# Kernel tuning notes

Hardware: AMD Instinct MI355X
Metric: run time of the kernel (lower is better)

## Reference

```python
import jax, jax.numpy as jnp
import numpy as np

LN_EPS = 1e-5


def _layer_norm(x, w, b, eps=LN_EPS):
    mu = jnp.mean(x, axis=-1, keepdims=True)
    var = jnp.var(x, axis=-1, keepdims=True)
    return (x - mu) * jax.lax.rsqrt(var + eps) * w + b


def setup_inputs() -> dict:
    key = jax.random.key(0)
    ks = jax.random.split(key, 6)
    H, I, B, S = 1024, 4096, 4, 2048
    return {
        "x": jax.random.normal(ks[0], (B, S, H), jnp.float32),
        "ln_weight": jnp.ones((H,), jnp.float32),
        "ln_bias": jnp.zeros((H,), jnp.float32),
        "i2h_weight": jax.random.normal(ks[1], (2 * I, H), jnp.float32) * 0.02,
        "i2h_bias": jax.random.normal(ks[2], (2 * I,), jnp.float32) * 0.02,
        "h2o_weight": jax.random.normal(ks[3], (H, I), jnp.float32) * 0.02,
        "h2o_bias": jax.random.normal(ks[4], (H,), jnp.float32) * 0.02,
        "post_ln_weight": jnp.ones((H,), jnp.float32),
        "post_ln_bias": jnp.zeros((H,), jnp.float32),
    }


def reference(x, ln_weight, ln_bias, i2h_weight, i2h_bias, h2o_weight, h2o_bias,
              post_ln_weight, post_ln_bias):
    B, S, H = x.shape
    x2 = x.reshape(-1, H)  # [N, H]
    x_ln = _layer_norm(x2, ln_weight, ln_bias)
    # i2h: [N, 2I]
    pre = jnp.einsum('nh,oh->no', x_ln, i2h_weight) + i2h_bias
    I = pre.shape[-1] // 2
    pre_gate, lin = pre[:, :I], pre[:, I:]
    # gated gelu (tanh-approx, matching gelu_fused)
    hid = jax.nn.gelu(pre_gate, approximate=True) * lin
    out = jnp.einsum('ni,oi->no', hid, h2o_weight) + h2o_bias
    out = _layer_norm(out, post_ln_weight, post_ln_bias)
    out = out + x2  # residual (dropout=0)
    return out.reshape(B, S, H)
```

## Files before the change

### kernel.cpp

```cpp
#include <hip/hip_runtime.h>
#include <stdint.h>

#define N_ROWS 8192
#define H_DIM  1024
#define I_DIM  4096

typedef unsigned short u16;
typedef __bf16 bf16x8 __attribute__((ext_vector_type(8)));
typedef float f32x4 __attribute__((ext_vector_type(4)));
typedef u16 u16x4 __attribute__((ext_vector_type(4)));

__device__ __forceinline__ u16 f2bf(float f) {
    union { float f; uint32_t u; } v; v.f = f;
    uint32_t u = v.u;
    u += 0x7FFFu + ((u >> 16) & 1u);
    return (u16)(u >> 16);
}

__device__ __forceinline__ float bf2f(u16 h) {
    union { uint32_t u; float f; } v; v.u = ((uint32_t)h) << 16;
    return v.f;
}

__device__ __forceinline__ float gelu_tanh(float x) {
    float u = 0.7978845608028654f * (x + 0.044715f * x * x * x);
    u = fminf(fmaxf(u, -15.f), 15.f);
    float e = __expf(2.f * u);
    float t = (e - 1.f) / (e + 1.f);
    return 0.5f * x * (1.f + t);
}

__device__ __forceinline__ void load_lds16(const void* g, void* l) {
    auto gp = reinterpret_cast<const __attribute__((address_space(1))) uint32_t*>(
        reinterpret_cast<uintptr_t>(g));
    auto lp = reinterpret_cast<__attribute__((address_space(3))) uint32_t*>(
        static_cast<uint32_t>(reinterpret_cast<uintptr_t>(l)));
    __builtin_amdgcn_global_load_lds(gp, lp, 16, 0, 0);
}

__device__ __forceinline__ void stage_tile(const u16* __restrict__ src, int stride,
                                           int row0, int k0, u16* lds, int t) {
#pragma unroll
    for (int i = 0; i < 2; ++i) {
        int r = i * 64 + (t >> 2);
        int s = t & 3;
        int ss = s ^ (r & 3);
        const u16* g = src + (size_t)(row0 + r) * stride + k0 + ss * 8;
        load_lds16(g, lds + i * 2048 + t * 8);
    }
}

__device__ __forceinline__ bf16x8 ld_frag(const u16* lds, int row, int g) {
    int slot = g ^ (row & 3);
    return *reinterpret_cast<const bf16x8*>(lds + row * 32 + slot * 8);
}

__global__ __launch_bounds__(256, 2) void gemm1_gated(
    const u16* __restrict__ A, const u16* __restrict__ W,
    const float* __restrict__ bias, u16* __restrict__ hid)
{
    __shared__ u16 As[2][128 * 32];
    __shared__ u16 Bg[2][128 * 32];
    __shared__ u16 Bl[2][128 * 32];
    const int t = threadIdx.x;
    const int lane = t & 63, wid = t >> 6;
    const int wm = wid >> 1, wn = wid & 1;
    const int row0 = blockIdx.y * 128, c0 = blockIdx.x * 128;
    const int g = lane >> 4, r16 = lane & 15;

    f32x4 accg[4][4] = {};
    f32x4 accl[4][4] = {};

    stage_tile(A, H_DIM, row0, 0, As[0], t);
    stage_tile(W, H_DIM, c0, 0, Bg[0], t);
    stage_tile(W, H_DIM, I_DIM + c0, 0, Bl[0], t);

    const int NT = H_DIM / 32;
    for (int kt = 0; kt < NT; ++kt) {
        const int cur = kt & 1;
        __syncthreads();
        if (kt + 1 < NT) {
            const int k0 = (kt + 1) * 32;
            stage_tile(A, H_DIM, row0, k0, As[cur ^ 1], t);
            stage_tile(W, H_DIM, c0, k0, Bg[cur ^ 1], t);
            stage_tile(W, H_DIM, I_DIM + c0, k0, Bl[cur ^ 1], t);
        }
        bf16x8 af[4], bgf[4], blf[4];
#pragma unroll
        for (int m = 0; m < 4; ++m) af[m] = ld_frag(As[cur], wm * 64 + m * 16 + r16, g);
#pragma unroll
        for (int n = 0; n < 4; ++n) {
            bgf[n] = ld_frag(Bg[cur], wn * 64 + n * 16 + r16, g);
            blf[n] = ld_frag(Bl[cur], wn * 64 + n * 16 + r16, g);
        }
#pragma unroll
        for (int m = 0; m < 4; ++m)
#pragma unroll
            for (int n = 0; n < 4; ++n) {
                accg[m][n] = __builtin_amdgcn_mfma_f32_16x16x32_bf16(af[m], bgf[n], accg[m][n], 0, 0, 0);
                accl[m][n] = __builtin_amdgcn_mfma_f32_16x16x32_bf16(af[m], blf[n], accl[m][n], 0, 0, 0);
            }
    }

#pragma unroll
    for (int m = 0; m < 4; ++m)
#pragma unroll
        for (int n = 0; n < 4; ++n) {
            const int cg = c0 + wn * 64 + n * 16 + r16;
            const float bgv = bias[cg], blv = bias[I_DIM + cg];
#pragma unroll
            for (int r = 0; r < 4; ++r) {
                const int row = row0 + wm * 64 + m * 16 + g * 4 + r;
                float gate = accg[m][n][r] + bgv;
                float lin  = accl[m][n][r] + blv;
                hid[(size_t)row * I_DIM + cg] = f2bf(gelu_tanh(gate) * lin);
            }
        }
}

__global__ __launch_bounds__(256, 2) void gemm2_k(
    const u16* __restrict__ A, const u16* __restrict__ W,
    const float* __restrict__ bias, u16* __restrict__ opb)
{
    __shared__ u16 As[2][128 * 32];
    __shared__ u16 Bs[2][128 * 32];
    const int t = threadIdx.x;
    const int lane = t & 63, wid = t >> 6;
    const int wm = wid >> 1, wn = wid & 1;
    const int row0 = blockIdx.y * 128, c0 = blockIdx.x * 128;
    const int g = lane >> 4, r16 = lane & 15;

    f32x4 acc[4][4] = {};

    stage_tile(A, I_DIM, row0, 0, As[0], t);
    stage_tile(W, I_DIM, c0, 0, Bs[0], t);

    const int NT = I_DIM / 32;
    for (int kt = 0; kt < NT; ++kt) {
        const int cur = kt & 1;
        __syncthreads();
        if (kt + 1 < NT) {
            const int k0 = (kt + 1) * 32;
            stage_tile(A, I_DIM, row0, k0, As[cur ^ 1], t);
            stage_tile(W, I_DIM, c0, k0, Bs[cur ^ 1], t);
        }
        bf16x8 af[4], bf[4];
#pragma unroll
        for (int m = 0; m < 4; ++m) af[m] = ld_frag(As[cur], wm * 64 + m * 16 + r16, g);
#pragma unroll
        for (int n = 0; n < 4; ++n) bf[n] = ld_frag(Bs[cur], wn * 64 + n * 16 + r16, g);
#pragma unroll
        for (int m = 0; m < 4; ++m)
#pragma unroll
            for (int n = 0; n < 4; ++n)
                acc[m][n] = __builtin_amdgcn_mfma_f32_16x16x32_bf16(af[m], bf[n], acc[m][n], 0, 0, 0);
    }

#pragma unroll
    for (int m = 0; m < 4; ++m)
#pragma unroll
        for (int n = 0; n < 4; ++n) {
            const int cg = c0 + wn * 64 + n * 16 + r16;
            const float bv = bias[cg];
#pragma unroll
            for (int r = 0; r < 4; ++r) {
                const int row = row0 + wm * 64 + m * 16 + g * 4 + r;
                opb[(size_t)row * H_DIM + cg] = f2bf(acc[m][n][r] + bv);
            }
        }
}

__device__ __forceinline__ void block_mean_var(float s, float s2, float* red, int t,
                                               float& mu, float& var) {
#pragma unroll
    for (int off = 32; off > 0; off >>= 1) {
        s  += __shfl_down(s, off);
        s2 += __shfl_down(s2, off);
    }
    const int wid = t >> 6;
    if ((t & 63) == 0) { red[wid] = s; red[4 + wid] = s2; }
    __syncthreads();
    if (t == 0) {
        float a = red[0] + red[1] + red[2] + red[3];
        float b = red[4] + red[5] + red[6] + red[7];
        red[0] = a * (1.f / H_DIM);
        red[1] = b * (1.f / H_DIM);
    }
    __syncthreads();
    mu = red[0];
    var = red[1] - mu * mu;
}

__global__ void ln_pre(const float* __restrict__ x, const float* __restrict__ w,
                       const float* __restrict__ b, u16* __restrict__ xln)
{
    __shared__ float red[8];
    const int row = blockIdx.x, t = threadIdx.x;
    const float4 v = reinterpret_cast<const float4*>(x + (size_t)row * H_DIM)[t];
    float mu, var;
    block_mean_var(v.x + v.y + v.z + v.w,
                   v.x * v.x + v.y * v.y + v.z * v.z + v.w * v.w, red, t, mu, var);
    const float rstd = rsqrtf(var + 1e-5f);
    const float4 wv = reinterpret_cast<const float4*>(w)[t];
    const float4 bv = reinterpret_cast<const float4*>(b)[t];
    u16x4 o;
    o.x = f2bf((v.x - mu) * rstd * wv.x + bv.x);
    o.y = f2bf((v.y - mu) * rstd * wv.y + bv.y);
    o.z = f2bf((v.z - mu) * rstd * wv.z + bv.z);
    o.w = f2bf((v.w - mu) * rstd * wv.w + bv.w);
    reinterpret_cast<u16x4*>(xln + (size_t)row * H_DIM)[t] = o;
}

__global__ void ln_post_res(const u16* __restrict__ op, const float* __restrict__ w,
                            const float* __restrict__ b, const float* __restrict__ x,
                            float* __restrict__ out)
{
    __shared__ float red[8];
    const int row = blockIdx.x, t = threadIdx.x;
    const u16x4 hv = reinterpret_cast<const u16x4*>(op + (size_t)row * H_DIM)[t];
    float4 v;
    v.x = bf2f(hv.x); v.y = bf2f(hv.y); v.z = bf2f(hv.z); v.w = bf2f(hv.w);
    float mu, var;
    block_mean_var(v.x + v.y + v.z + v.w,
                   v.x * v.x + v.y * v.y + v.z * v.z + v.w * v.w, red, t, mu, var);
    const float rstd = rsqrtf(var + 1e-5f);
    const float4 wv = reinterpret_cast<const float4*>(w)[t];
    const float4 bv = reinterpret_cast<const float4*>(b)[t];
    const float4 xv = reinterpret_cast<const float4*>(x + (size_t)row * H_DIM)[t];
    float4 o;
    o.x = (v.x - mu) * rstd * wv.x + bv.x + xv.x;
    o.y = (v.y - mu) * rstd * wv.y + bv.y + xv.y;
    o.z = (v.z - mu) * rstd * wv.z + bv.z + xv.z;
    o.w = (v.w - mu) * rstd * wv.w + bv.w + xv.w;
    reinterpret_cast<float4*>(out + (size_t)row * H_DIM)[t] = o;
}

__global__ void cvt_bf16(const float* __restrict__ in, u16* __restrict__ out, int n4) {
    int i = blockIdx.x * blockDim.x + threadIdx.x;
    if (i >= n4) return;
    float4 v = reinterpret_cast<const float4*>(in)[i];
    u16x4 o = { f2bf(v.x), f2bf(v.y), f2bf(v.z), f2bf(v.w) };
    reinterpret_cast<u16x4*>(out)[i] = o;
}

extern "C" void kernel_launch(void* const* d_in, const int* in_sizes, int n_in,
                              void* d_out, int out_size, void* d_ws, size_t ws_size,
                              hipStream_t stream)
{
    const float* x   = (const float*)d_in[0];
    const float* lnw = (const float*)d_in[1];
    const float* lnb = (const float*)d_in[2];
    const float* w1  = (const float*)d_in[3];
    const float* b1  = (const float*)d_in[4];
    const float* w2  = (const float*)d_in[5];
    const float* b2  = (const float*)d_in[6];
    const float* pw  = (const float*)d_in[7];
    const float* pb  = (const float*)d_in[8];
    float* out = (float*)d_out;

    char* ws = (char*)d_ws;
    u16* xln = (u16*)(ws);
    u16* w1b = (u16*)(ws + (16u << 20));
    u16* hid = (u16*)(ws + (32u << 20));
    u16* w2b = (u16*)(ws);
    u16* opb = (u16*)(ws + (8u << 20));

    cvt_bf16<<<(2 * I_DIM * H_DIM / 4 + 255) / 256, 256, 0, stream>>>(w1, w1b, 2 * I_DIM * H_DIM / 4);
    ln_pre<<<N_ROWS, 256, 0, stream>>>(x, lnw, lnb, xln);
    gemm1_gated<<<dim3(I_DIM / 128, N_ROWS / 128), 256, 0, stream>>>(xln, w1b, b1, hid);
    cvt_bf16<<<(H_DIM * I_DIM / 4 + 255) / 256, 256, 0, stream>>>(w2, w2b, H_DIM * I_DIM / 4);
    gemm2_k<<<dim3(H_DIM / 128, N_ROWS / 128), 256, 0, stream>>>(hid, w2b, b2, opb);
    ln_post_res<<<N_ROWS, 256, 0, stream>>>(opb, pw, pb, x, out);
}
```

Measured before the change: 274.2 us.

## Restructure both GEMMs with 256-row tiles, triple-buffered LDS and interleaved MFMA phases

Both GEMM kernels move to 256x128 block tiles. GEMM1 uses 512 threads and GEMM2 keeps 256 threads with larger per-wave tiles. A three-slot LDS ring prefetches two k-steps ahead, and each iteration is split into four phases that interleave single global-to-LDS loads with MFMA batches, using explicit barriers, waitcnt and setprio. Block IDs are remapped to group neighbouring tiles for L2 reuse, and the swizzle pattern changes. The goal is to hide load latency and raise MFMA utilisation, at the cost of much more hand-scheduled synchronisation and fewer blocks for GEMM2 (256).

```diff
diff --git a/kernel.cpp b/kernel.cpp
--- a/kernel.cpp
+++ b/kernel.cpp
@@ -9,6 +9,12 @@
 typedef __bf16 bf16x8 __attribute__((ext_vector_type(8)));
 typedef float f32x4 __attribute__((ext_vector_type(4)));
 typedef u16 u16x4 __attribute__((ext_vector_type(4)));
+
+#define BAR()   asm volatile("s_barrier" ::: "memory")
+#define LGKM0() do { asm volatile("s_waitcnt lgkmcnt(0)" ::: "memory"); __builtin_amdgcn_sched_barrier(0); } while (0)
+#define VMW4()  do { asm volatile("s_waitcnt vmcnt(4)" ::: "memory"); __builtin_amdgcn_sched_barrier(0); } while (0)
+#define VMW6()  do { asm volatile("s_waitcnt vmcnt(6)" ::: "memory"); __builtin_amdgcn_sched_barrier(0); } while (0)
+#define VMW0()  do { asm volatile("s_waitcnt vmcnt(0)" ::: "memory"); __builtin_amdgcn_sched_barrier(0); } while (0)
 
 __device__ __forceinline__ u16 f2bf(float f) {
     union { float f; uint32_t u; } v; v.f = f;
@@ -38,136 +44,239 @@
     __builtin_amdgcn_global_load_lds(gp, lp, 16, 0, 0);
 }
 
-__device__ __forceinline__ void stage_tile(const u16* __restrict__ src, int stride,
-                                           int row0, int k0, u16* lds, int t) {
-#pragma unroll
-    for (int i = 0; i < 2; ++i) {
-        int r = i * 64 + (t >> 2);
-        int s = t & 3;
-        int ss = s ^ (r & 3);
-        const u16* g = src + (size_t)(row0 + r) * stride + k0 + ss * 8;
-        load_lds16(g, lds + i * 2048 + t * 8);
-    }
-}
-
-__device__ __forceinline__ bf16x8 ld_frag(const u16* lds, int row, int g) {
-    int slot = g ^ (row & 3);
-    return *reinterpret_cast<const bf16x8*>(lds + row * 32 + slot * 8);
-}
-
-__global__ __launch_bounds__(256, 2) void gemm1_gated(
+__global__ __launch_bounds__(512, 2) void gemm1_gated(
     const u16* __restrict__ A, const u16* __restrict__ W,
     const float* __restrict__ bias, u16* __restrict__ hid)
 {
-    __shared__ u16 As[2][128 * 32];
-    __shared__ u16 Bg[2][128 * 32];
-    __shared__ u16 Bl[2][128 * 32];
+    __shared__ u16 lds[3 * 16384];
+    const int t = threadIdx.x;
+    const int lane = t & 63, wid = t >> 6;
+    const int wm = wid >> 2, wn = wid & 3;
+    const int g = lane >> 4, r16 = lane & 15;
+
+    int bid = blockIdx.x;
+    bid = (bid & 7) * 128 + (bid >> 3);
+    const int brow = (bid >> 5) * 256;
+    const int bcol = (bid & 31) * 128;
+
+    const int tr = t >> 2, ts = t & 3;
+    const int tswz = ts ^ ((tr >> 1) & 3);
+    const u16* pA  = A + (size_t)(brow + tr) * H_DIM + tswz * 8;
+    const u16* pBg = W + (size_t)(bcol + tr) * H_DIM + tswz * 8;
+    const u16* pBl = W + (size_t)(I_DIM + bcol + tr) * H_DIM + tswz * 8;
+    const int dst = t * 8;
+
+    const int sRd   = (g ^ ((r16 >> 1) & 3)) * 8;
+    const int offA  = (wm * 128 + r16) * 32 + sRd;
+    const int offBg = (wn * 32 + r16) * 32 + sRd;
+    const int offBl = offBg + 4096;
+
+    f32x4 accg[8][2] = {};
+    f32x4 accl[8][2] = {};
+
+#pragma unroll
+    for (int p = 0; p < 2; ++p) {
+        u16* dA = lds + p * 16384; u16* dB = dA + 8192;
+        load_lds16(pA + p * 32,                 dA + dst);
+        load_lds16(pA + 128 * H_DIM + p * 32,   dA + 4096 + dst);
+        load_lds16(pBg + p * 32,                dB + dst);
+        load_lds16(pBl + p * 32,                dB + 4096 + dst);
+    }
+    VMW4(); BAR();
+
+    int slot = 0, s2 = 2;
+    for (int kt = 0; kt < 32; ++kt) {
+        const u16* lA = lds + slot * 16384;
+        const u16* lB = lA + 8192;
+        u16* dA = lds + s2 * 16384;
+        u16* dB = dA + 8192;
+        const bool st = (kt + 2 < 32);
+        const int k2 = (kt + 2) * 32;
+        bf16x8 af[4], bg[2], bl[2];
+
+        if (st) load_lds16(pA + k2, dA + dst);
+#pragma unroll
+        for (int m = 0; m < 4; ++m) af[m] = *(const bf16x8*)(lA + offA + m * 512);
+#pragma unroll
+        for (int n = 0; n < 2; ++n) bg[n] = *(const bf16x8*)(lB + offBg + n * 512);
+        BAR(); LGKM0(); __builtin_amdgcn_s_setprio(1);
+#pragma unroll
+        for (int m = 0; m < 4; ++m)
+#pragma unroll
+            for (int n = 0; n < 2; ++n)
+                accg[m][n] = __builtin_amdgcn_mfma_f32_16x16x32_bf16(af[m], bg[n], accg[m][n], 0, 0, 0);
+        __builtin_amdgcn_s_setprio(0); BAR();
+
+        if (st) load_lds16(pA + 128 * H_DIM + k2, dA + 4096 + dst);
+#pragma unroll
+        for (int n = 0; n < 2; ++n) bl[n] = *(const bf16x8*)(lB + offBl + n * 512);
+        BAR(); LGKM0(); __builtin_amdgcn_s_setprio(1);
+#pragma unroll
+        for (int m = 0; m < 4; ++m)
+#pragma unroll
+            for (int n = 0; n < 2; ++n)
+                accl[m][n] = __builtin_amdgcn_mfma_f32_16x16x32_bf16(af[m], bl[n], accl[m][n], 0, 0, 0);
+        __builtin_amdgcn_s_setprio(0); BAR();
+
+        if (st) load_lds16(pBg + k2, dB + dst);
+#pragma unroll
+        for (int m = 0; m < 4; ++m) af[m] = *(const bf16x8*)(lA + offA + (m + 4) * 512);
+        BAR(); LGKM0(); __builtin_amdgcn_s_setprio(1);
+#pragma unroll
+        for (int m = 0; m < 4; ++m)
+#pragma unroll
+            for (int n = 0; n < 2; ++n)
+                accl[m + 4][n] = __builtin_amdgcn_mfma_f32_16x16x32_bf16(af[m], bl[n], accl[m + 4][n], 0, 0, 0);
+        __builtin_amdgcn_s_setprio(0); BAR();
+
+        if (st) load_lds16(pBl + k2, dB + 4096 + dst);
+        BAR(); __builtin_amdgcn_s_setprio(1);
+#pragma unroll
+        for (int m = 0; m < 4; ++m)
+#pragma unroll
+            for (int n = 0; n < 2; ++n)
+                accg[m + 4][n] = __builtin_amdgcn_mfma_f32_16x16x32_bf16(af[m], bg[n], accg[m + 4][n], 0, 0, 0);
+        __builtin_amdgcn_s_setprio(0);
+        if (st) { VMW4(); } else { VMW0(); }
+        BAR();
+        slot = (slot == 2) ? 0 : slot + 1;
+        s2   = (s2 == 2) ? 0 : s2 + 1;
+    }
+
+#pragma unroll
+    for (int n = 0; n < 2; ++n) {
+        const int cg = bcol + wn * 32 + n * 16 + r16;
+        const float bgv = bias[cg], blv = bias[I_DIM + cg];
+#pragma unroll
+        for (int m = 0; m < 8; ++m) {
+            const int row = brow + wm * 128 + m * 16 + g * 4;
+            u16* hp = hid + (size_t)row * I_DIM + cg;
+#pragma unroll
+            for (int r = 0; r < 4; ++r) {
+                float gate = accg[m][n][r] + bgv;
+                float lin  = accl[m][n][r] + blv;
+                hp[(size_t)r * I_DIM] = f2bf(gelu_tanh(gate) * lin);
+            }
+        }
+    }
+}
+
+__global__ __launch_bounds__(256, 2) void gemm2_k(
+    const u16* __restrict__ A, const u16* __restrict__ W,
+    const float* __restrict__ bias, u16* __restrict__ opb)
+{
+    __shared__ u16 lds[3 * 12288];
     const int t = threadIdx.x;
     const int lane = t & 63, wid = t >> 6;
     const int wm = wid >> 1, wn = wid & 1;
-    const int row0 = blockIdx.y * 128, c0 = blockIdx.x * 128;
     const int g = lane >> 4, r16 = lane & 15;
 
-    f32x4 accg[4][4] = {};
-    f32x4 accl[4][4] = {};
-
-    stage_tile(A, H_DIM, row0, 0, As[0], t);
-    stage_tile(W, H_DIM, c0, 0, Bg[0], t);
-    stage_tile(W, H_DIM, I_DIM + c0, 0, Bl[0], t);
-
-    const int NT = H_DIM / 32;
-    for (int kt = 0; kt < NT; ++kt) {
-        const int cur = kt & 1;
-        __syncthreads();
-        if (kt + 1 < NT) {
-            const int k0 = (kt + 1) * 32;
-            stage_tile(A, H_DIM, row0, k0, As[cur ^ 1], t);
-            stage_tile(W, H_DIM, c0, k0, Bg[cur ^ 1], t);
-            stage_tile(W, H_DIM, I_DIM + c0, k0, Bl[cur ^ 1], t);
+    int bid = blockIdx.x;
+    bid = (bid & 7) * 32 + (bid >> 3);
+    const int brow = (bid >> 3) * 256;
+    const int bcol = (bid & 7) * 128;
+
+    const int tr = t >> 2, ts = t & 3;
+    const int tswz = ts ^ ((tr >> 1) & 3);
+    const u16* pA = A + (size_t)(brow + tr) * I_DIM + tswz * 8;
+    const u16* pB = W + (size_t)(bcol + tr) * I_DIM + tswz * 8;
+    const int dst = t * 8;
+
+    const int sRd  = (g ^ ((r16 >> 1) & 3)) * 8;
+    const int offA = (wm * 128 + r16) * 32 + sRd;
+    const int offB = 8192 + (wn * 64 + r16) * 32 + sRd;
+
+    f32x4 acc[8][4] = {};
+
+#pragma unroll
+    for (int p = 0; p < 2; ++p) {
+        u16* dA = lds + p * 12288; u16* dB = dA + 8192;
+#pragma unroll
+        for (int i = 0; i < 4; ++i)
+            load_lds16(pA + (size_t)i * 64 * I_DIM + p * 32, dA + i * 2048 + dst);
+#pragma unroll
+        for (int i = 0; i < 2; ++i)
+            load_lds16(pB + (size_t)i * 64 * I_DIM + p * 32, dB + i * 2048 + dst);
+    }
+    VMW6(); BAR();
+
+    int slot = 0, s2 = 2;
+    for (int kt = 0; kt < 128; ++kt) {
+        const u16* lA = lds + slot * 12288;
+        u16* dA = lds + s2 * 12288;
+        u16* dB = dA + 8192;
+        const bool st = (kt + 2 < 128);
+        const int k2 = (kt + 2) * 32;
+        bf16x8 af[4], bf[4];
+
+        if (st) {
+            load_lds16(pA + k2, dA + dst);
+            load_lds16(pA + (size_t)64 * I_DIM + k2, dA + 2048 + dst);
         }
-        bf16x8 af[4], bgf[4], blf[4];
-#pragma unroll
-        for (int m = 0; m < 4; ++m) af[m] = ld_frag(As[cur], wm * 64 + m * 16 + r16, g);
-#pragma unroll
-        for (int n = 0; n < 4; ++n) {
-            bgf[n] = ld_frag(Bg[cur], wn * 64 + n * 16 + r16, g);
-            blf[n] = ld_frag(Bl[cur], wn * 64 + n * 16 + r16, g);
+#pragma unroll
+        for (int m = 0; m < 4; ++m) af[m] = *(const bf16x8*)(lA + offA + m * 512);
+#pragma unroll
+        for (int n = 0; n < 2; ++n) bf[n] = *(const bf16x8*)(lA + offB + n * 512);
+        BAR(); LGKM0(); __builtin_amdgcn_s_setprio(1);
+#pragma unroll
+        for (int m = 0; m < 4; ++m)
+#pragma unroll
+            for (int n = 0; n < 2; ++n)
+                acc[m][n] = __builtin_amdgcn_mfma_f32_16x16x32_bf16(af[m], bf[n], acc[m][n], 0, 0, 0);
+        __builtin_amdgcn_s_setprio(0); BAR();
+
+        if (st) {
+            load_lds16(pA + (size_t)128 * I_DIM + k2, dA + 4096 + dst);
+            load_lds16(pA + (size_t)192 * I_DIM + k2, dA + 6144 + dst);
         }
 #pragma unroll
-        for (int m = 0; m < 4; ++m)
-#pragma unroll
-            for (int n = 0; n < 4; ++n) {
-                accg[m][n] = __builtin_amdgcn_mfma_f32_16x16x32_bf16(af[m], bgf[n], accg[m][n], 0, 0, 0);
-                accl[m][n] = __builtin_amdgcn_mfma_f32_16x16x32_bf16(af[m], blf[n], accl[m][n], 0, 0, 0);
-            }
-    }
-
-#pragma unroll
-    for (int m = 0; m < 4; ++m)
-#pragma unroll
-        for (int n = 0; n < 4; ++n) {
-            const int cg = c0 + wn * 64 + n * 16 + r16;
-            const float bgv = bias[cg], blv = bias[I_DIM + cg];
-#pragma unroll
-            for (int r = 0; r < 4; ++r) {
-                const int row = row0 + wm * 64 + m * 16 + g * 4 + r;
-                float gate = accg[m][n][r] + bgv;
-                float lin  = accl[m][n][r] + blv;
-                hid[(size_t)row * I_DIM + cg] = f2bf(gelu_tanh(gate) * lin);
-            }
+        for (int n = 2; n < 4; ++n) bf[n] = *(const bf16x8*)(lA + offB + n * 512);
+        BAR(); LGKM0(); __builtin_amdgcn_s_setprio(1);
+#pragma unroll
+        for (int m = 0; m < 4; ++m)
+#pragma unroll
+            for (int n = 2; n < 4; ++n)
+                acc[m][n] = __builtin_amdgcn_mfma_f32_16x16x32_bf16(af[m], bf[n], acc[m][n], 0, 0, 0);
+        __builtin_amdgcn_s_setprio(0); BAR();
+
+        if (st) load_lds16(pB + k2, dB + dst);
+#pragma unroll
+        for (int m = 0; m < 4; ++m) af[m] = *(const bf16x8*)(lA + offA + (m + 4) * 512);
+        BAR(); LGKM0(); __builtin_amdgcn_s_setprio(1);
+#pragma unroll
+        for (int m = 0; m < 4; ++m)
+#pragma unroll
+            for (int n = 2; n < 4; ++n)
+                acc[m + 4][n] = __builtin_amdgcn_mfma_f32_16x16x32_bf16(af[m], bf[n], acc[m + 4][n], 0, 0, 0);
+        __builtin_amdgcn_s_setprio(0); BAR();
+
+        if (st) load_lds16(pB + (size_t)64 * I_DIM + k2, dB + 2048 + dst);
+        BAR(); __builtin_amdgcn_s_setprio(1);
+#pragma unroll
+        for (int m = 0; m < 4; ++m)
+#pragma unroll
+            for (int n = 0; n < 2; ++n)
+                acc[m + 4][n] = __builtin_amdgcn_mfma_f32_16x16x32_bf16(af[m], bf[n], acc[m + 4][n], 0, 0, 0);
+        __builtin_amdgcn_s_setprio(0);
+        if (st) { VMW6(); } else { VMW0(); }
+        BAR();
+        slot = (slot == 2) ? 0 : slot + 1;
+        s2   = (s2 == 2) ? 0 : s2 + 1;
+    }
+
+#pragma unroll
+    for (int n = 0; n < 4; ++n) {
+        const int cg = bcol + wn * 64 + n * 16 + r16;
+        const float bv = bias[cg];
+#pragma unroll
+        for (int m = 0; m < 8; ++m) {
+            const int row = brow + wm * 128 + m * 16 + g * 4;
+            u16* op = opb + (size_t)row * H_DIM + cg;
+#pragma unroll
+            for (int r = 0; r < 4; ++r)
+                op[(size_t)r * H_DIM] = f2bf(acc[m][n][r] + bv);
         }
-}
-
-__global__ __launch_bounds__(256, 2) void gemm2_k(
-    const u16* __restrict__ A, const u16* __restrict__ W,
-    const float* __restrict__ bias, u16* __restrict__ opb)
-{
-    __shared__ u16 As[2][128 * 32];
-    __shared__ u16 Bs[2][128 * 32];
-    const int t = threadIdx.x;
-    const int lane = t & 63, wid = t >> 6;
-    const int wm = wid >> 1, wn = wid & 1;
-    const int row0 = blockIdx.y * 128, c0 = blockIdx.x * 128;
-    const int g = lane >> 4, r16 = lane & 15;
-
-    f32x4 acc[4][4] = {};
-
-    stage_tile(A, I_DIM, row0, 0, As[0], t);
-    stage_tile(W, I_DIM, c0, 0, Bs[0], t);
-
-    const int NT = I_DIM / 32;
-    for (int kt = 0; kt < NT; ++kt) {
-        const int cur = kt & 1;
-        __syncthreads();
-        if (kt + 1 < NT) {
-            const int k0 = (kt + 1) * 32;
-            stage_tile(A, I_DIM, row0, k0, As[cur ^ 1], t);
-            stage_tile(W, I_DIM, c0, k0, Bs[cur ^ 1], t);
-        }
-        bf16x8 af[4], bf[4];
-#pragma unroll
-        for (int m = 0; m < 4; ++m) af[m] = ld_frag(As[cur], wm * 64 + m * 16 + r16, g);
-#pragma unroll
-        for (int n = 0; n < 4; ++n) bf[n] = ld_frag(Bs[cur], wn * 64 + n * 16 + r16, g);
-#pragma unroll
-        for (int m = 0; m < 4; ++m)
-#pragma unroll
-            for (int n = 0; n < 4; ++n)
-                acc[m][n] = __builtin_amdgcn_mfma_f32_16x16x32_bf16(af[m], bf[n], acc[m][n], 0, 0, 0);
-    }
-
-#pragma unroll
-    for (int m = 0; m < 4; ++m)
-#pragma unroll
-        for (int n = 0; n < 4; ++n) {
-            const int cg = c0 + wn * 64 + n * 16 + r16;
-            const float bv = bias[cg];
-#pragma unroll
-            for (int r = 0; r < 4; ++r) {
-                const int row = row0 + wm * 64 + m * 16 + g * 4 + r;
-                opb[(size_t)row * H_DIM + cg] = f2bf(acc[m][n][r] + bv);
-            }
-        }
+    }
 }
 
 __device__ __forceinline__ void block_mean_var(float s, float s2, float* red, int t,
@@ -267,8 +376,8 @@
 
     cvt_bf16<<<(2 * I_DIM * H_DIM / 4 + 255) / 256, 256, 0, stream>>>(w1, w1b, 2 * I_DIM * H_DIM / 4);
     ln_pre<<<N_ROWS, 256, 0, stream>>>(x, lnw, lnb, xln);
-    gemm1_gated<<<dim3(I_DIM / 128, N_ROWS / 128), 256, 0, stream>>>(xln, w1b, b1, hid);
+    gemm1_gated<<<1024, 512, 0, stream>>>(xln, w1b, b1, hid);
     cvt_bf16<<<(H_DIM * I_DIM / 4 + 255) / 256, 256, 0, stream>>>(w2, w2b, H_DIM * I_DIM / 4);
-    gemm2_k<<<dim3(H_DIM / 128, N_ROWS / 128), 256, 0, stream>>>(hid, w2b, b2, opb);
+    gemm2_k<<<256, 256, 0, stream>>>(hid, w2b, b2, opb);
     ln_post_res<<<N_ROWS, 256, 0, stream>>>(opb, pw, pb, x, out);
 }
```

After: 288.0 us. +5.0%, slower.

## Restructure both GEMMs into 256x128 tiles with 8 waves and finer-grained pipelining

Applied to the files above, without the earlier changes.

Both GEMM kernels move from 128x128 tiles with 4 waves to 256-row by 128-column tiles with 8 waves (512 threads), and use a K step of 64 split into two 32-wide substages. Explicit vmcnt/lgkmcnt waits, raw s_barrier and s_setprio around the MFMA block replace __syncthreads so the next tile's global-to-LDS loads overlap the current MFMAs. A new XOR swizzle is applied to the LDS layout. The aim is more data reuse per block and better hiding of memory latency, at the cost of larger LDS use, higher register pressure and fragile hand-placed wait counts.

```diff
diff --git a/kernel.cpp b/kernel.cpp
--- a/kernel.cpp
+++ b/kernel.cpp
@@ -9,6 +9,10 @@
 typedef __bf16 bf16x8 __attribute__((ext_vector_type(8)));
 typedef float f32x4 __attribute__((ext_vector_type(4)));
 typedef u16 u16x4 __attribute__((ext_vector_type(4)));
+
+#define BAR()   asm volatile("s_barrier" ::: "memory")
+#define LGKM0() do { asm volatile("s_waitcnt lgkmcnt(0)" ::: "memory"); __builtin_amdgcn_sched_barrier(0); } while (0)
+#define VMW(n)  do { asm volatile("s_waitcnt vmcnt(" #n ")" ::: "memory"); __builtin_amdgcn_sched_barrier(0); } while (0)
 
 __device__ __forceinline__ u16 f2bf(float f) {
     union { float f; uint32_t u; } v; v.f = f;
@@ -38,136 +42,179 @@
     __builtin_amdgcn_global_load_lds(gp, lp, 16, 0, 0);
 }
 
-__device__ __forceinline__ void stage_tile(const u16* __restrict__ src, int stride,
-                                           int row0, int k0, u16* lds, int t) {
-#pragma unroll
-    for (int i = 0; i < 2; ++i) {
-        int r = i * 64 + (t >> 2);
-        int s = t & 3;
-        int ss = s ^ (r & 3);
-        const u16* g = src + (size_t)(row0 + r) * stride + k0 + ss * 8;
-        load_lds16(g, lds + i * 2048 + t * 8);
-    }
-}
-
-__device__ __forceinline__ bf16x8 ld_frag(const u16* lds, int row, int g) {
-    int slot = g ^ (row & 3);
-    return *reinterpret_cast<const bf16x8*>(lds + row * 32 + slot * 8);
-}
-
-__global__ __launch_bounds__(256, 2) void gemm1_gated(
+__global__ __launch_bounds__(512, 2) void gemm1_gated(
     const u16* __restrict__ A, const u16* __restrict__ W,
     const float* __restrict__ bias, u16* __restrict__ hid)
 {
-    __shared__ u16 As[2][128 * 32];
-    __shared__ u16 Bg[2][128 * 32];
-    __shared__ u16 Bl[2][128 * 32];
+    __shared__ u16 lds[2 * 32768];
+    const int t = threadIdx.x;
+    const int lane = t & 63, wid = t >> 6;
+    const int wm = wid >> 2, wn = wid & 3;
+    const int g = lane >> 4, r16 = lane & 15;
+
+    const int brow = blockIdx.y * 256;
+    const int bcol = blockIdx.x * 128;
+
+    const int tr = t >> 2;
+    const int swz8 = ((t & 3) ^ ((t >> 3) & 3)) * 8;
+    const u16* pA  = A + (size_t)(brow + tr) * H_DIM + swz8;
+    const u16* pBg = W + (size_t)(bcol + tr) * H_DIM + swz8;
+    const u16* pBl = W + (size_t)(I_DIM + bcol + tr) * H_DIM + swz8;
+    const int dst = t * 8;
+
+    const int sl    = (g ^ ((r16 >> 1) & 3)) * 8;
+    const int rdA   = (wm * 128 + r16) * 32 + sl;
+    const int rdBg  = 16384 + (wn * 32 + r16) * 32 + sl;
+    const int rdBl  = rdBg + 4096;
+
+    f32x4 accg[8][2] = {};
+    f32x4 accl[8][2] = {};
+
+#pragma unroll
+    for (int s = 0; s < 2; ++s) {
+        load_lds16(pA + s * 32,                 lds + s * 8192 + dst);
+        load_lds16(pA + 128 * H_DIM + s * 32,   lds + s * 8192 + 4096 + dst);
+        load_lds16(pBg + s * 32,                lds + 16384 + s * 8192 + dst);
+        load_lds16(pBl + s * 32,                lds + 16384 + s * 8192 + 4096 + dst);
+    }
+    VMW(4); BAR();
+
+    const int NT = H_DIM / 64;
+    for (int kt = 0; kt < NT; ++kt) {
+        const u16* lA = lds + (kt & 1) * 32768;
+        u16* dS = lds + ((kt & 1) ^ 1) * 32768;
+        const bool st = (kt + 1 < NT);
+        const int k1 = (kt + 1) * 64;
+        const bool tail = (kt == NT - 1);
+
+#pragma unroll
+        for (int ks = 0; ks < 2; ++ks) {
+            bf16x8 af[8], bg[2], bl[2];
+#pragma unroll
+            for (int m = 0; m < 8; ++m) af[m] = *(const bf16x8*)(lA + ks * 8192 + rdA + m * 512);
+#pragma unroll
+            for (int n = 0; n < 2; ++n) {
+                bg[n] = *(const bf16x8*)(lA + ks * 8192 + rdBg + n * 512);
+                bl[n] = *(const bf16x8*)(lA + ks * 8192 + rdBl + n * 512);
+            }
+            if (st) {
+                load_lds16(pA + k1 + ks * 32,               dS + ks * 8192 + dst);
+                load_lds16(pA + 128 * H_DIM + k1 + ks * 32, dS + ks * 8192 + 4096 + dst);
+                load_lds16(pBg + k1 + ks * 32,              dS + 16384 + ks * 8192 + dst);
+                load_lds16(pBl + k1 + ks * 32,              dS + 16384 + ks * 8192 + 4096 + dst);
+            }
+            if (tail) { VMW(0); } else { VMW(4); }
+            BAR(); LGKM0();
+            __builtin_amdgcn_s_setprio(1);
+#pragma unroll
+            for (int m = 0; m < 8; ++m)
+#pragma unroll
+                for (int n = 0; n < 2; ++n) {
+                    accg[m][n] = __builtin_amdgcn_mfma_f32_16x16x32_bf16(af[m], bg[n], accg[m][n], 0, 0, 0);
+                    accl[m][n] = __builtin_amdgcn_mfma_f32_16x16x32_bf16(af[m], bl[n], accl[m][n], 0, 0, 0);
+                }
+            __builtin_amdgcn_s_setprio(0);
+            BAR();
+        }
+    }
+
+#pragma unroll
+    for (int n = 0; n < 2; ++n) {
+        const int cg = bcol + wn * 32 + n * 16 + r16;
+        const float bgv = bias[cg], blv = bias[I_DIM + cg];
+#pragma unroll
+        for (int m = 0; m < 8; ++m) {
+            const int row = brow + wm * 128 + m * 16 + g * 4;
+            u16* hp = hid + (size_t)row * I_DIM + cg;
+#pragma unroll
+            for (int r = 0; r < 4; ++r) {
+                float gate = accg[m][n][r] + bgv;
+                float lin  = accl[m][n][r] + blv;
+                hp[(size_t)r * I_DIM] = f2bf(gelu_tanh(gate) * lin);
+            }
+        }
+    }
+}
+
+__global__ __launch_bounds__(512, 2) void gemm2_k(
+    const u16* __restrict__ A, const u16* __restrict__ W,
+    const float* __restrict__ bias, u16* __restrict__ opb)
+{
+    __shared__ u16 lds[2 * 24576];
     const int t = threadIdx.x;
     const int lane = t & 63, wid = t >> 6;
     const int wm = wid >> 1, wn = wid & 1;
-    const int row0 = blockIdx.y * 128, c0 = blockIdx.x * 128;
     const int g = lane >> 4, r16 = lane & 15;
 
-    f32x4 accg[4][4] = {};
-    f32x4 accl[4][4] = {};
-
-    stage_tile(A, H_DIM, row0, 0, As[0], t);
-    stage_tile(W, H_DIM, c0, 0, Bg[0], t);
-    stage_tile(W, H_DIM, I_DIM + c0, 0, Bl[0], t);
-
-    const int NT = H_DIM / 32;
+    const int brow = blockIdx.y * 256;
+    const int bcol = blockIdx.x * 128;
+
+    const int tr = t >> 2;
+    const int swz8 = ((t & 3) ^ ((t >> 3) & 3)) * 8;
+    const u16* pA = A + (size_t)(brow + tr) * I_DIM + swz8;
+    const u16* pB = W + (size_t)(bcol + tr) * I_DIM + swz8;
+    const int dst = t * 8;
+
+    const int sl   = (g ^ ((r16 >> 1) & 3)) * 8;
+    const int rdA  = (wm * 64 + r16) * 32 + sl;
+    const int rdB  = 16384 + (wn * 64 + r16) * 32 + sl;
+
+    f32x4 acc[4][4] = {};
+
+#pragma unroll
+    for (int s = 0; s < 2; ++s) {
+        load_lds16(pA + s * 32,               lds + s * 8192 + dst);
+        load_lds16(pA + 128 * I_DIM + s * 32, lds + s * 8192 + 4096 + dst);
+        load_lds16(pB + s * 32,               lds + 16384 + s * 4096 + dst);
+    }
+    VMW(3); BAR();
+
+    const int NT = I_DIM / 64;
     for (int kt = 0; kt < NT; ++kt) {
-        const int cur = kt & 1;
-        __syncthreads();
-        if (kt + 1 < NT) {
-            const int k0 = (kt + 1) * 32;
-            stage_tile(A, H_DIM, row0, k0, As[cur ^ 1], t);
-            stage_tile(W, H_DIM, c0, k0, Bg[cur ^ 1], t);
-            stage_tile(W, H_DIM, I_DIM + c0, k0, Bl[cur ^ 1], t);
+        const u16* lA = lds + (kt & 1) * 24576;
+        u16* dS = lds + ((kt & 1) ^ 1) * 24576;
+        const bool st = (kt + 1 < NT);
+        const int k1 = (kt + 1) * 64;
+        const bool tail = (kt == NT - 1);
+
+#pragma unroll
+        for (int ks = 0; ks < 2; ++ks) {
+            bf16x8 af[4], bf[4];
+#pragma unroll
+            for (int m = 0; m < 4; ++m) af[m] = *(const bf16x8*)(lA + ks * 8192 + rdA + m * 512);
+#pragma unroll
+            for (int n = 0; n < 4; ++n) bf[n] = *(const bf16x8*)(lA + ks * 4096 + rdB + n * 512);
+            if (st) {
+                load_lds16(pA + k1 + ks * 32,               dS + ks * 8192 + dst);
+                load_lds16(pA + 128 * I_DIM + k1 + ks * 32, dS + ks * 8192 + 4096 + dst);
+                load_lds16(pB + k1 + ks * 32,               dS + 16384 + ks * 4096 + dst);
+            }
+            if (tail) { VMW(0); } else { VMW(3); }
+            BAR(); LGKM0();
+            __builtin_amdgcn_s_setprio(1);
+#pragma unroll
+            for (int m = 0; m < 4; ++m)
+#pragma unroll
+                for (int n = 0; n < 4; ++n)
+                    acc[m][n] = __builtin_amdgcn_mfma_f32_16x16x32_bf16(af[m], bf[n], acc[m][n], 0, 0, 0);
+            __builtin_amdgcn_s_setprio(0);
+            BAR();
         }
-        bf16x8 af[4], bgf[4], blf[4];
-#pragma unroll
-        for (int m = 0; m < 4; ++m) af[m] = ld_frag(As[cur], wm * 64 + m * 16 + r16, g);
-#pragma unroll
-        for (int n = 0; n < 4; ++n) {
-            bgf[n] = ld_frag(Bg[cur], wn * 64 + n * 16 + r16, g);
-            blf[n] = ld_frag(Bl[cur], wn * 64 + n * 16 + r16, g);
+    }
+
+#pragma unroll
+    for (int n = 0; n < 4; ++n) {
+        const int cg = bcol + wn * 64 + n * 16 + r16;
+        const float bv = bias[cg];
+#pragma unroll
+        for (int m = 0; m < 4; ++m) {
+            const int row = brow + wm * 64 + m * 16 + g * 4;
+            u16* op = opb + (size_t)row * H_DIM + cg;
+#pragma unroll
+            for (int r = 0; r < 4; ++r)
+                op[(size_t)r * H_DIM] = f2bf(acc[m][n][r] + bv);
         }
-#pragma unroll
-        for (int m = 0; m < 4; ++m)
-#pragma unroll
-            for (int n = 0; n < 4; ++n) {
-                accg[m][n] = __builtin_amdgcn_mfma_f32_16x16x32_bf16(af[m], bgf[n], accg[m][n], 0, 0, 0);
-                accl[m][n] = __builtin_amdgcn_mfma_f32_16x16x32_bf16(af[m], blf[n], accl[m][n], 0, 0, 0);
-            }
-    }
-
-#pragma unroll
-    for (int m = 0; m < 4; ++m)
-#pragma unroll
-        for (int n = 0; n < 4; ++n) {
-            const int cg = c0 + wn * 64 + n * 16 + r16;
-            const float bgv = bias[cg], blv = bias[I_DIM + cg];
-#pragma unroll
-            for (int r = 0; r < 4; ++r) {
-                const int row = row0 + wm * 64 + m * 16 + g * 4 + r;
-                float gate = accg[m][n][r] + bgv;
-                float lin  = accl[m][n][r] + blv;
-                hid[(size_t)row * I_DIM + cg] = f2bf(gelu_tanh(gate) * lin);
-            }
-        }
-}
-
-__global__ __launch_bounds__(256, 2) void gemm2_k(
-    const u16* __restrict__ A, const u16* __restrict__ W,
-    const float* __restrict__ bias, u16* __restrict__ opb)
-{
-    __shared__ u16 As[2][128 * 32];
-    __shared__ u16 Bs[2][128 * 32];
-    const int t = threadIdx.x;
-    const int lane = t & 63, wid = t >> 6;
-    const int wm = wid >> 1, wn = wid & 1;
-    const int row0 = blockIdx.y * 128, c0 = blockIdx.x * 128;
-    const int g = lane >> 4, r16 = lane & 15;
-
-    f32x4 acc[4][4] = {};
-
-    stage_tile(A, I_DIM, row0, 0, As[0], t);
-    stage_tile(W, I_DIM, c0, 0, Bs[0], t);
-
-    const int NT = I_DIM / 32;
-    for (int kt = 0; kt < NT; ++kt) {
-        const int cur = kt & 1;
-        __syncthreads();
-        if (kt + 1 < NT) {
-            const int k0 = (kt + 1) * 32;
-            stage_tile(A, I_DIM, row0, k0, As[cur ^ 1], t);
-            stage_tile(W, I_DIM, c0, k0, Bs[cur ^ 1], t);
-        }
-        bf16x8 af[4], bf[4];
-#pragma unroll
-        for (int m = 0; m < 4; ++m) af[m] = ld_frag(As[cur], wm * 64 + m * 16 + r16, g);
-#pragma unroll
-        for (int n = 0; n < 4; ++n) bf[n] = ld_frag(Bs[cur], wn * 64 + n * 16 + r16, g);
-#pragma unroll
-        for (int m = 0; m < 4; ++m)
-#pragma unroll
-            for (int n = 0; n < 4; ++n)
-                acc[m][n] = __builtin_amdgcn_mfma_f32_16x16x32_bf16(af[m], bf[n], acc[m][n], 0, 0, 0);
-    }
-
-#pragma unroll
-    for (int m = 0; m < 4; ++m)
-#pragma unroll
-        for (int n = 0; n < 4; ++n) {
-            const int cg = c0 + wn * 64 + n * 16 + r16;
-            const float bv = bias[cg];
-#pragma unroll
-            for (int r = 0; r < 4; ++r) {
-                const int row = row0 + wm * 64 + m * 16 + g * 4 + r;
-                opb[(size_t)row * H_DIM + cg] = f2bf(acc[m][n][r] + bv);
-            }
-        }
+    }
 }
 
 __device__ __forceinline__ void block_mean_var(float s, float s2, float* red, int t,
@@ -267,8 +314,8 @@
 
     cvt_bf16<<<(2 * I_DIM * H_DIM / 4 + 255) / 256, 256, 0, stream>>>(w1, w1b, 2 * I_DIM * H_DIM / 4);
     ln_pre<<<N_ROWS, 256, 0, stream>>>(x, lnw, lnb, xln);
-    gemm1_gated<<<dim3(I_DIM / 128, N_ROWS / 128), 256, 0, stream>>>(xln, w1b, b1, hid);
+    gemm1_gated<<<dim3(I_DIM / 128, N_ROWS / 256), 512, 0, stream>>>(xln, w1b, b1, hid);
     cvt_bf16<<<(H_DIM * I_DIM / 4 + 255) / 256, 256, 0, stream>>>(w2, w2b, H_DIM * I_DIM / 4);
-    gemm2_k<<<dim3(H_DIM / 128, N_ROWS / 128), 256, 0, stream>>>(hid, w2b, b2, opb);
+    gemm2_k<<<dim3(H_DIM / 128, N_ROWS / 256), 512, 0, stream>>>(hid, w2b, b2, opb);
     ln_post_res<<<N_ROWS, 256, 0, stream>>>(opb, pw, pb, x, out);
 }
```

Result: no change. 276.9 us (+1.0%).
